# Optimization experiments

Measured on AMD Instinct MI355X. Metric: run time of the kernel, lower is better.

The kernel has to match this reference:

```python
import jax, jax.numpy as jnp
import numpy as np

N, C_IN, C_OUT, H, W = 16, 256, 256, 32, 32
K = 9  # 3x3 kernel


def setup_inputs() -> dict:
    key = jax.random.key(0)
    k1, k2, k3 = jax.random.split(key, 3)
    x = jax.random.normal(k1, (N, C_IN, H, W), dtype=jnp.float32)
    # offsets as produced upstream from anchors: (N, H*W, 18)
    offset = jax.random.normal(k2, (N, H * W, 2 * K), dtype=jnp.float32)
    # DeformConv weight (no bias), kaiming-ish scale
    weight = jax.random.normal(k3, (C_OUT, C_IN, 3, 3), dtype=jnp.float32) * 0.02
    return {"x": x, "offset": offset, "weight": weight}


def _deform_conv3x3(x, offset_nchw, weight):
    """DeformConv v1, kernel 3x3, stride 1, padding 1, dilation 1,
    groups=1, deformable_groups=1, zero padding outside borders."""
    n, c, h, w = x.shape
    o = weight.shape[0]
    # offset channel layout: (dy_k, dx_k) pairs for k = 0..8
    off = offset_nchw.reshape(n, K, 2, h, w)
    dy = off[:, :, 0]  # (N,K,H,W)
    dx = off[:, :, 1]
    ky = (jnp.arange(K) // 3 - 1).astype(x.dtype)  # kernel row offsets -1,0,1
    kx = (jnp.arange(K) % 3 - 1).astype(x.dtype)
    base_y = jnp.arange(h, dtype=x.dtype)[None, None, :, None]
    base_x = jnp.arange(w, dtype=x.dtype)[None, None, None, :]
    py = base_y + ky[None, :, None, None] + dy  # (N,K,H,W) sample rows
    px = base_x + kx[None, :, None, None] + dx  # (N,K,H,W) sample cols

    y0 = jnp.floor(py)
    x0 = jnp.floor(px)
    ly = py - y0  # fractional parts
    lx = px - x0

    x_flat = x.reshape(n, c, h * w)

    def corner(yi, xi, wgt):
        valid = (yi >= 0) & (yi <= h - 1) & (xi >= 0) & (xi <= w - 1)
        yc = jnp.clip(yi, 0, h - 1).astype(jnp.int32)
        xc = jnp.clip(xi, 0, w - 1).astype(jnp.int32)
        idx = (yc * w + xc).reshape(n, K * h * w)
        g = jax.vmap(lambda xf, i: xf[:, i])(x_flat, idx)  # (N,C,K*H*W)
        wv = (wgt * valid.astype(x.dtype)).reshape(n, 1, K * h * w)
        return g * wv

    val = (corner(y0, x0, (1 - ly) * (1 - lx))
           + corner(y0, x0 + 1, (1 - ly) * lx)
           + corner(y0 + 1, x0, ly * (1 - lx))
           + corner(y0 + 1, x0 + 1, ly * lx))
    val = val.reshape(n, c, K, h, w)  # sampled im2col columns
    return jnp.einsum('nckhw,ock->nohw', val, weight.reshape(o, c, K))


def reference(x, offset, weight):
    n, _, h, w = x.shape
    assert h * w == offset.shape[1]
    # AdaptiveConv.forward: (N, HW, 18) -> (N, 18, H, W)
    offset_nchw = jnp.transpose(offset, (0, 2, 1)).reshape(n, 2 * K, h, w)
    return _deform_conv3x3(x, offset_nchw, weight)
```

## Files before the change

### kernel.cpp

```cpp
#include <hip/hip_runtime.h>

#define NB   16
#define CIN  256
#define COUT 256
#define HH   32
#define WW   32
#define HW   1024
#define KK   9
#define CK   2304

typedef __bf16 bf16x8 __attribute__((ext_vector_type(8)));
typedef float  f32x4  __attribute__((ext_vector_type(4)));

__device__ __forceinline__ unsigned short f2bf(float f) {
    unsigned int u = __float_as_uint(f);
    u += 0x7FFFu + ((u >> 16) & 1u);
    return (unsigned short)(u >> 16);
}
__device__ __forceinline__ float bfhi(unsigned int u) {
    return __uint_as_float(u & 0xFFFF0000u);
}
__device__ __forceinline__ float bflo(unsigned int u) {
    return __uint_as_float(u << 16);
}

typedef const __attribute__((address_space(1))) void* gas_ptr;
typedef __attribute__((address_space(3))) void* las_ptr;

__device__ __forceinline__ void async16(const void* g, void* l) {
    __builtin_amdgcn_global_load_lds((gas_ptr)g, (las_ptr)l, 16, 0, 0);
}

__global__ __launch_bounds__(256) void wconv_kernel(const float* __restrict__ w,
                                                    unsigned short* __restrict__ wbf) {
    __shared__ float ls[CK];
    const int o = blockIdx.x;
    const float* wo = w + (size_t)o * CK;
#pragma unroll
    for (int i = threadIdx.x; i < CK; i += 256) ls[i] = wo[i];
    __syncthreads();
    unsigned short* dst = wbf + (size_t)o * CK;
#pragma unroll
    for (int i = threadIdx.x; i < CK; i += 256) {
        int k = i >> 8, c = i & 255;
        dst[i] = f2bf(ls[c * KK + k]);
    }
}

__global__ __launch_bounds__(256) void xt_kernel(const float* __restrict__ x,
                                                 unsigned short* __restrict__ xtb) {
    __shared__ float ls[64][65];
    const int c0  = blockIdx.x * 64;
    const int hw0 = blockIdx.y * 64;
    const int n   = blockIdx.z;
    const int t   = threadIdx.x;
    {
        int c = t >> 2, q = t & 3;
        const float* base = x + ((size_t)(n * CIN + c0 + c)) * HW + hw0 + q * 16;
#pragma unroll
        for (int j = 0; j < 16; ++j) ls[c][q * 16 + j] = base[j];
    }
    __syncthreads();
    {
        int hw = t >> 2, seg = (t & 3) * 16;
        unsigned int dw[8];
#pragma unroll
        for (int j = 0; j < 8; ++j) {
            float f0 = ls[seg + 2 * j][hw];
            float f1 = ls[seg + 2 * j + 1][hw];
            dw[j] = (unsigned)f2bf(f0) | ((unsigned)f2bf(f1) << 16);
        }
        uint4* dst = (uint4*)(xtb + ((size_t)(n * HW + hw0 + hw)) * CIN + c0 + seg);
        dst[0] = *(uint4*)&dw[0];
        dst[1] = *(uint4*)&dw[4];
    }
}

__global__ __launch_bounds__(512, 2) void fused_kernel(const unsigned short* __restrict__ wbf,
                                                       const unsigned short* __restrict__ xtb,
                                                       const float* __restrict__ off,
                                                       float* __restrict__ out) {
    __shared__ unsigned short As[256 * 64];
    __shared__ unsigned short Bs[64 * 64];

    const int tid  = threadIdx.x;
    const int wv   = tid >> 6;
    const int lane = tid & 63;
    const int quad = lane >> 4;
    const int l15  = lane & 15;

    const int hw_local = tid >> 3;
    const int seg      = tid & 7;

    const int id  = blockIdx.x;
    const int hw0 = (id & 15) * 64;
    const int n   = id >> 4;

    const int hw = hw0 + hw_local;
    const int h  = hw >> 5, w = hw & 31;

    const int srow   = lane >> 3;
    const int schunk = (lane & 7) ^ (srow & 7);

    const uint4*  xb4  = (const uint4*)(xtb + (size_t)n * HW * CIN);
    const float2* offp = (const float2*)(off + ((size_t)n * HW + hw) * (2 * KK));

    f32x4 acc[2][4] = {};

    for (int tap = 0; tap < KK; ++tap) {
        float2 o = offp[tap];
        float py = (float)(h + tap / 3 - 1) + o.x;
        float px = (float)(w + tap % 3 - 1) + o.y;
        float y0f = floorf(py), x0f = floorf(px);
        float ly = py - y0f, lx = px - x0f;
        int y0 = (int)y0f, x0 = (int)x0f;

        float wg[4];
        int   ix[4];
#pragma unroll
        for (int c2 = 0; c2 < 4; ++c2) {
            int yy = y0 + (c2 >> 1);
            int xx = x0 + (c2 & 1);
            float wy = (c2 >> 1) ? ly : 1.0f - ly;
            float wx = (c2 & 1) ? lx : 1.0f - lx;
            bool v = (yy >= 0) && (yy < HH) && (xx >= 0) && (xx < WW);
            wg[c2] = v ? wy * wx : 0.0f;
            int yc = yy < 0 ? 0 : (yy > HH - 1 ? HH - 1 : yy);
            int xc = xx < 0 ? 0 : (xx > WW - 1 ? WW - 1 : xx);
            ix[c2] = yc * WW + xc;
        }

        uint4 cr[4][4];
#pragma unroll
        for (int c2 = 0; c2 < 4; ++c2) {
            const uint4* rp = xb4 + (size_t)ix[c2] * 32 + seg;
#pragma unroll
            for (int s = 0; s < 4; ++s) cr[c2][s] = rp[s * 8];
        }

#pragma unroll
        for (int s = 0; s < 4; ++s) {
            __syncthreads();

            const int ckb = tap * 256 + s * 64;
#pragma unroll
            for (int j = 0; j < 4; ++j) {
                int rb = wv * 32 + j * 8;
                async16(wbf + (size_t)(rb + srow) * CK + ckb + schunk * 8,
                        &As[rb * 64]);
            }

            unsigned dw[4];
            {
                unsigned u0[4], u1[4], u2[4], u3[4];
                *(uint4*)u0 = cr[0][s]; *(uint4*)u1 = cr[1][s];
                *(uint4*)u2 = cr[2][s]; *(uint4*)u3 = cr[3][s];
#pragma unroll
                for (int d = 0; d < 4; ++d) {
                    float lo = wg[0] * bflo(u0[d]) + wg[1] * bflo(u1[d])
                             + wg[2] * bflo(u2[d]) + wg[3] * bflo(u3[d]);
                    float hi = wg[0] * bfhi(u0[d]) + wg[1] * bfhi(u1[d])
                             + wg[2] * bfhi(u2[d]) + wg[3] * bfhi(u3[d]);
                    dw[d] = (unsigned)f2bf(lo) | ((unsigned)f2bf(hi) << 16);
                }
            }
            *(uint4*)&Bs[hw_local * 64 + (seg ^ (hw_local & 7)) * 8] = *(uint4*)dw;

            __syncthreads();

            bf16x8 af[2][2], bfr[4][2];
#pragma unroll
            for (int mi = 0; mi < 2; ++mi)
#pragma unroll
                for (int hh = 0; hh < 2; ++hh) {
                    int row = wv * 32 + mi * 16 + l15;
                    int ch  = (hh * 4 + quad) ^ (row & 7);
                    af[mi][hh] = *(const bf16x8*)&As[row * 64 + ch * 8];
                }
#pragma unroll
            for (int ni = 0; ni < 4; ++ni)
#pragma unroll
                for (int hh = 0; hh < 2; ++hh) {
                    int row = ni * 16 + l15;
                    int ch  = (hh * 4 + quad) ^ (row & 7);
                    bfr[ni][hh] = *(const bf16x8*)&Bs[row * 64 + ch * 8];
                }
#pragma unroll
            for (int mi = 0; mi < 2; ++mi)
#pragma unroll
                for (int ni = 0; ni < 4; ++ni) {
                    acc[mi][ni] = __builtin_amdgcn_mfma_f32_16x16x32_bf16(af[mi][0], bfr[ni][0], acc[mi][ni], 0, 0, 0);
                    acc[mi][ni] = __builtin_amdgcn_mfma_f32_16x16x32_bf16(af[mi][1], bfr[ni][1], acc[mi][ni], 0, 0, 0);
                }
        }
    }

    float* opnt = out + (size_t)n * COUT * HW + hw0;
#pragma unroll
    for (int mi = 0; mi < 2; ++mi)
#pragma unroll
        for (int ni = 0; ni < 4; ++ni) {
            int col = ni * 16 + l15;
#pragma unroll
            for (int rr = 0; rr < 4; ++rr) {
                int row = wv * 32 + mi * 16 + quad * 4 + rr;
                opnt[(size_t)row * HW + col] = acc[mi][ni][rr];
            }
        }
}

extern "C" void kernel_launch(void* const* d_in, const int* in_sizes, int n_in,
                              void* d_out, int out_size, void* d_ws, size_t ws_size,
                              hipStream_t stream) {
    const float* x   = (const float*)d_in[0];
    const float* off = (const float*)d_in[1];
    const float* wt  = (const float*)d_in[2];
    float* out = (float*)d_out;

    unsigned short* wbf = (unsigned short*)d_ws;
    unsigned short* xtb = (unsigned short*)((char*)d_ws + 1179648);

    wconv_kernel<<<256, 256, 0, stream>>>(wt, wbf);
    xt_kernel<<<dim3(4, 16, 16), 256, 0, stream>>>(x, xtb);
    fused_kernel<<<256, 512, 0, stream>>>(wbf, xtb, off, out);
}
```

Measured before the change: 132.3 us.

## Double-buffer LDS tiles and pipeline gather/build with MFMA steps

Splits the A and B shared tiles into two buffers so the next k-slice's weight async load and bilinear-sampled B tile are built while MFMAs consume the current buffer. This cuts the barriers per slice from two to one and prefetches the next tap's corner gathers. Block-to-(n,hw) mapping is also remapped so that block ids consecutive within each group of 16 cover different batches. The cost is doubled LDS use (now about 80 KB per block), which may limit occupancy at two blocks per CU.

```diff
diff --git a/kernel.cpp b/kernel.cpp
--- a/kernel.cpp
+++ b/kernel.cpp
@@ -80,8 +80,8 @@
                                                        const unsigned short* __restrict__ xtb,
                                                        const float* __restrict__ off,
                                                        float* __restrict__ out) {
-    __shared__ unsigned short As[256 * 64];
-    __shared__ unsigned short Bs[64 * 64];
+    __shared__ unsigned short As[2][256 * 64];
+    __shared__ unsigned short Bs[2][64 * 64];
 
     const int tid  = threadIdx.x;
     const int wv   = tid >> 6;
@@ -93,8 +93,8 @@
     const int seg      = tid & 7;
 
     const int id  = blockIdx.x;
-    const int hw0 = (id & 15) * 64;
-    const int n   = id >> 4;
+    const int n   = ((id & 7) << 1) | ((id >> 3) & 1);
+    const int hw0 = (id >> 4) * 64;
 
     const int hw = hw0 + hw_local;
     const int h  = hw >> 5, w = hw & 31;
@@ -107,16 +107,13 @@
 
     f32x4 acc[2][4] = {};
 
-    for (int tap = 0; tap < KK; ++tap) {
+    auto setup = [&](int tap, float wg[4], int ix[4]) {
         float2 o = offp[tap];
         float py = (float)(h + tap / 3 - 1) + o.x;
         float px = (float)(w + tap % 3 - 1) + o.y;
         float y0f = floorf(py), x0f = floorf(px);
         float ly = py - y0f, lx = px - x0f;
         int y0 = (int)y0f, x0 = (int)x0f;
-
-        float wg[4];
-        int   ix[4];
 #pragma unroll
         for (int c2 = 0; c2 < 4; ++c2) {
             int yy = y0 + (c2 >> 1);
@@ -129,69 +126,93 @@
             int xc = xx < 0 ? 0 : (xx > WW - 1 ? WW - 1 : xx);
             ix[c2] = yc * WW + xc;
         }
-
-        uint4 cr[4][4];
-#pragma unroll
-        for (int c2 = 0; c2 < 4; ++c2) {
-            const uint4* rp = xb4 + (size_t)ix[c2] * 32 + seg;
-#pragma unroll
-            for (int s = 0; s < 4; ++s) cr[c2][s] = rp[s * 8];
-        }
-
-#pragma unroll
-        for (int s = 0; s < 4; ++s) {
+    };
+
+    auto loadc = [&](uint4 cr[4], const int ix[4], int s) {
+#pragma unroll
+        for (int c2 = 0; c2 < 4; ++c2)
+            cr[c2] = xb4[(size_t)ix[c2] * 32 + s * 8 + seg];
+    };
+
+    auto build = [&](int nb, int ckb, const uint4 cr[4], const float wg[4]) {
+        unsigned u0[4], u1[4], u2[4], u3[4];
+        *(uint4*)u0 = cr[0]; *(uint4*)u1 = cr[1];
+        *(uint4*)u2 = cr[2]; *(uint4*)u3 = cr[3];
+        unsigned dw[4];
+#pragma unroll
+        for (int d = 0; d < 4; ++d) {
+            float lo = wg[0] * bflo(u0[d]) + wg[1] * bflo(u1[d])
+                     + wg[2] * bflo(u2[d]) + wg[3] * bflo(u3[d]);
+            float hi = wg[0] * bfhi(u0[d]) + wg[1] * bfhi(u1[d])
+                     + wg[2] * bfhi(u2[d]) + wg[3] * bfhi(u3[d]);
+            dw[d] = (unsigned)f2bf(lo) | ((unsigned)f2bf(hi) << 16);
+        }
+        *(uint4*)&Bs[nb][hw_local * 64 + (seg ^ (hw_local & 7)) * 8] = *(uint4*)dw;
+#pragma unroll
+        for (int j = 0; j < 4; ++j) {
+            int rb = wv * 32 + j * 8;
+            async16(wbf + (size_t)(rb + srow) * CK + ckb + schunk * 8, &As[nb][rb * 64]);
+        }
+    };
+
+    auto mfma_step = [&](int pb) {
+        bf16x8 af[2][2], bfr[4][2];
+#pragma unroll
+        for (int mi = 0; mi < 2; ++mi)
+#pragma unroll
+            for (int hh = 0; hh < 2; ++hh) {
+                int row = wv * 32 + mi * 16 + l15;
+                int ch  = (hh * 4 + quad) ^ (row & 7);
+                af[mi][hh] = *(const bf16x8*)&As[pb][row * 64 + ch * 8];
+            }
+#pragma unroll
+        for (int ni = 0; ni < 4; ++ni)
+#pragma unroll
+            for (int hh = 0; hh < 2; ++hh) {
+                int row = ni * 16 + l15;
+                int ch  = (hh * 4 + quad) ^ (row & 7);
+                bfr[ni][hh] = *(const bf16x8*)&Bs[pb][row * 64 + ch * 8];
+            }
+#pragma unroll
+        for (int mi = 0; mi < 2; ++mi)
+#pragma unroll
+            for (int ni = 0; ni < 4; ++ni) {
+                acc[mi][ni] = __builtin_amdgcn_mfma_f32_16x16x32_bf16(af[mi][0], bfr[ni][0], acc[mi][ni], 0, 0, 0);
+                acc[mi][ni] = __builtin_amdgcn_mfma_f32_16x16x32_bf16(af[mi][1], bfr[ni][1], acc[mi][ni], 0, 0, 0);
+            }
+    };
+
+    float wgc[4], wgn[4];
+    int   ixc[4], ixn[4];
+    uint4 crA[4], crB[4];
+
+    setup(0, wgc, ixc);
+    loadc(crA, ixc, 0);
+    build(0, 0, crA, wgc);
+    loadc(crB, ixc, 1);
+    __syncthreads();
+
+    for (int tap = 0; tap < 9; ++tap) {
+        const int ckb = tap * 256;
+        mfma_step(0);
+        build(1, ckb + 64, crB, wgc);
+        loadc(crA, ixc, 2);
+        __syncthreads();
+        mfma_step(1);
+        build(0, ckb + 128, crA, wgc);
+        loadc(crB, ixc, 3);
+        __syncthreads();
+        mfma_step(0);
+        build(1, ckb + 192, crB, wgc);
+        if (tap < 8) { setup(tap + 1, wgn, ixn); loadc(crA, ixn, 0); }
+        __syncthreads();
+        mfma_step(1);
+        if (tap < 8) {
+            build(0, ckb + 256, crA, wgn);
+            loadc(crB, ixn, 1);
+#pragma unroll
+            for (int c2 = 0; c2 < 4; ++c2) { wgc[c2] = wgn[c2]; ixc[c2] = ixn[c2]; }
             __syncthreads();
-
-            const int ckb = tap * 256 + s * 64;
-#pragma unroll
-            for (int j = 0; j < 4; ++j) {
-                int rb = wv * 32 + j * 8;
-                async16(wbf + (size_t)(rb + srow) * CK + ckb + schunk * 8,
-                        &As[rb * 64]);
-            }
-
-            unsigned dw[4];
-            {
-                unsigned u0[4], u1[4], u2[4], u3[4];
-                *(uint4*)u0 = cr[0][s]; *(uint4*)u1 = cr[1][s];
-                *(uint4*)u2 = cr[2][s]; *(uint4*)u3 = cr[3][s];
-#pragma unroll
-                for (int d = 0; d < 4; ++d) {
-                    float lo = wg[0] * bflo(u0[d]) + wg[1] * bflo(u1[d])
-                             + wg[2] * bflo(u2[d]) + wg[3] * bflo(u3[d]);
-                    float hi = wg[0] * bfhi(u0[d]) + wg[1] * bfhi(u1[d])
-                             + wg[2] * bfhi(u2[d]) + wg[3] * bfhi(u3[d]);
-                    dw[d] = (unsigned)f2bf(lo) | ((unsigned)f2bf(hi) << 16);
-                }
-            }
-            *(uint4*)&Bs[hw_local * 64 + (seg ^ (hw_local & 7)) * 8] = *(uint4*)dw;
-
-            __syncthreads();
-
-            bf16x8 af[2][2], bfr[4][2];
-#pragma unroll
-            for (int mi = 0; mi < 2; ++mi)
-#pragma unroll
-                for (int hh = 0; hh < 2; ++hh) {
-                    int row = wv * 32 + mi * 16 + l15;
-                    int ch  = (hh * 4 + quad) ^ (row & 7);
-                    af[mi][hh] = *(const bf16x8*)&As[row * 64 + ch * 8];
-                }
-#pragma unroll
-            for (int ni = 0; ni < 4; ++ni)
-#pragma unroll
-                for (int hh = 0; hh < 2; ++hh) {
-                    int row = ni * 16 + l15;
-                    int ch  = (hh * 4 + quad) ^ (row & 7);
-                    bfr[ni][hh] = *(const bf16x8*)&Bs[row * 64 + ch * 8];
-                }
-#pragma unroll
-            for (int mi = 0; mi < 2; ++mi)
-#pragma unroll
-                for (int ni = 0; ni < 4; ++ni) {
-                    acc[mi][ni] = __builtin_amdgcn_mfma_f32_16x16x32_bf16(af[mi][0], bfr[ni][0], acc[mi][ni], 0, 0, 0);
-                    acc[mi][ni] = __builtin_amdgcn_mfma_f32_16x16x32_bf16(af[mi][1], bfr[ni][1], acc[mi][ni], 0, 0, 0);
-                }
         }
     }
 
```

New measurement: 125.4 us. 1.06x faster.
